# Optimization experiments

Measured on AMD Instinct MI355X. Metric: run time of the kernel, lower is better.

The kernel has to match this reference:

```python
import jax, jax.numpy as jnp
import numpy as np


def setup_inputs() -> dict:
    key = jax.random.key(0)
    k1, k2, k3 = jax.random.split(key, 3)
    B, M, J = 4096, 64, 24  # batch, n_max_markers, n_joints
    points = jax.random.normal(k1, (B, M, 3), dtype=jnp.float32)
    weight = jax.random.uniform(k2, (B, M, J), dtype=jnp.float32)  # positive soft weights
    offset = jax.random.normal(k3, (B, M, J, 3), dtype=jnp.float32)
    return {"points": points, "weight": weight, "offset": offset}


def reference(points, weight, offset):
    # P: per-joint marker offsets (B, J, 3, M); Q: world marker positions (B, 1, 3, M)
    P = jnp.transpose(offset, (0, 2, 3, 1))
    Q = jnp.transpose(points, (0, 2, 1))[:, None]
    w = jnp.transpose(weight, (0, 2, 1))[:, :, None]  # (B, J, 1, M)

    wsum = jnp.sum(w, axis=-1)                   # (B, J, 1)
    P_ = jnp.sum(P * w, axis=-1) / wsum          # (B, J, 3) weighted centroid of offsets
    Q_ = jnp.sum(Q * w, axis=-1) / wsum          # (B, J, 3) weighted centroid of markers

    X = P - P_[..., None]                        # (B, J, 3, M)
    Y = Q - Q_[..., None]                        # (B, J, 3, M) via broadcast

    # Cross-covariance S = X @ Y^T (NOTE: original multiplies un-weighted centered coords)
    S = jnp.einsum('bjdm,bjem->bjde', X, Y)      # (B, J, 3, 3)

    U, _, Vh = jnp.linalg.svd(S)
    V = jnp.swapaxes(Vh, -1, -2)
    Ut = jnp.swapaxes(U, -1, -2)
    det = jnp.linalg.det(jnp.matmul(V, Ut))      # (B, J) reflection correction
    Ut = Ut.at[..., -1, :].multiply(det[..., None])
    R = jnp.matmul(V, Ut)                        # (B, J, 3, 3) optimal rotation
    t = Q_[..., None] - jnp.matmul(R, P_[..., None])  # (B, J, 3, 1)
    return R, t
```

## Files before the change

### kernel.cpp

```cpp
#include <hip/hip_runtime.h>


constexpr int M = 64;
constexpr int J = 24;
constexpr int NACC = 22;
constexpr int NWS  = 15;
constexpr int WPB  = 2;

template<int P, int Q>
__device__ __forceinline__ void jrot(float A[4][4], float V[4][4]) {
    float apq = A[P][Q];
    float theta = (A[Q][Q] - A[P][P]) * __builtin_amdgcn_rcpf(2.0f * apq);
    float t = __builtin_amdgcn_rcpf(fabsf(theta) + __builtin_amdgcn_sqrtf(fmaf(theta, theta, 1.0f)));
    t = (theta < 0.0f) ? -t : t;
    t = (apq == 0.0f) ? 0.0f : t;
    float c = __builtin_amdgcn_rsqf(fmaf(t, t, 1.0f));
    float s = t * c;
#pragma unroll
    for (int k = 0; k < 4; ++k) {
        float akp = A[k][P], akq = A[k][Q];
        A[k][P] = c * akp - s * akq;
        A[k][Q] = s * akp + c * akq;
    }
#pragma unroll
    for (int k = 0; k < 4; ++k) {
        float apk = A[P][k], aqk = A[Q][k];
        A[P][k] = c * apk - s * aqk;
        A[Q][k] = s * apk + c * aqk;
        float vkp = V[k][P], vkq = V[k][Q];
        V[k][P] = c * vkp - s * vkq;
        V[k][Q] = s * vkp + c * vkq;
    }
}

__device__ __forceinline__ void horn_solve(
    float S00, float S01, float S02, float S10, float S11, float S12,
    float S20, float S21, float S22,
    float cP0, float cP1, float cP2, float cQ0, float cQ1, float cQ2,
    float* __restrict__ Rout, float* __restrict__ tout)
{
    float A[4][4], V[4][4];
    A[0][0] = S00 + S11 + S22;
    A[0][1] = A[1][0] = S12 - S21;
    A[0][2] = A[2][0] = S20 - S02;
    A[0][3] = A[3][0] = S01 - S10;
    A[1][1] = S00 - S11 - S22;
    A[1][2] = A[2][1] = S01 + S10;
    A[1][3] = A[3][1] = S02 + S20;
    A[2][2] = -S00 + S11 - S22;
    A[2][3] = A[3][2] = S12 + S21;
    A[3][3] = -S00 - S11 + S22;
#pragma unroll
    for (int r = 0; r < 4; ++r)
#pragma unroll
        for (int c = 0; c < 4; ++c)
            V[r][c] = (r == c) ? 1.0f : 0.0f;

#pragma unroll 1
    for (int sweep = 0; sweep < 6; ++sweep) {
        jrot<0, 1>(A, V); jrot<0, 2>(A, V); jrot<0, 3>(A, V);
        jrot<1, 2>(A, V); jrot<1, 3>(A, V); jrot<2, 3>(A, V);
    }

    float best = A[0][0];
    float qw = V[0][0], qx = V[1][0], qy = V[2][0], qz = V[3][0];
#pragma unroll
    for (int i = 1; i < 4; ++i) {
        bool better = A[i][i] > best;
        best = better ? A[i][i] : best;
        qw = better ? V[0][i] : qw;
        qx = better ? V[1][i] : qx;
        qy = better ? V[2][i] : qy;
        qz = better ? V[3][i] : qz;
    }
    float nrm = __builtin_amdgcn_rsqf(qw * qw + qx * qx + qy * qy + qz * qz);
    qw *= nrm; qx *= nrm; qy *= nrm; qz *= nrm;

    float R00 = 1.f - 2.f * (qy * qy + qz * qz);
    float R01 = 2.f * (qx * qy - qw * qz);
    float R02 = 2.f * (qx * qz + qw * qy);
    float R10 = 2.f * (qx * qy + qw * qz);
    float R11 = 1.f - 2.f * (qx * qx + qz * qz);
    float R12 = 2.f * (qy * qz - qw * qx);
    float R20 = 2.f * (qx * qz - qw * qy);
    float R21 = 2.f * (qy * qz + qw * qx);
    float R22 = 1.f - 2.f * (qx * qx + qy * qy);

    Rout[0] = R00; Rout[1] = R01; Rout[2] = R02;
    Rout[3] = R10; Rout[4] = R11; Rout[5] = R12;
    Rout[6] = R20; Rout[7] = R21; Rout[8] = R22;
    tout[0] = cQ0 - (R00 * cP0 + R01 * cP1 + R02 * cP2);
    tout[1] = cQ1 - (R10 * cP0 + R11 * cP1 + R12 * cP2);
    tout[2] = cQ2 - (R20 * cP0 + R21 * cP1 + R22 * cP2);
}

__global__ __launch_bounds__(128, 4) void kabsch_fused(
    const float* __restrict__ points,
    const float* __restrict__ weight,
    const float* __restrict__ offset,
    float* __restrict__ out,
    int B, int bj_total)
{
    const int t    = threadIdx.x;
    const int wv   = t >> 6;
    const int lane = t & 63;
    const int jj   = lane >> 1;
    const int kk   = lane & 1;

    int bw = blockIdx.x * WPB + wv;
    bw = bw < B ? bw : B - 1;

    __shared__ float sv_s[WPB][NWS][J + 1];

    if (jj < J) {
        const float* wq = weight + (size_t)bw * (M * J) + (size_t)(kk * 32) * J + jj;
        const float* oq = offset + (size_t)bw * (M * J * 3) + (size_t)(kk * 32) * (J * 3) + jj * 3;
        const float* pq = points + (size_t)bw * (M * 3) + (size_t)(kk * 32) * 3;

        float acc[NACC];
#pragma unroll
        for (int n = 0; n < NACC; ++n) acc[n] = 0.0f;

#pragma unroll
        for (int i = 0; i < M / 2; ++i) {
            float w  = wq[i * J];
            float o0 = oq[i * 72 + 0];
            float o1 = oq[i * 72 + 1];
            float o2 = oq[i * 72 + 2];
            float p0 = pq[i * 3 + 0];
            float p1 = pq[i * 3 + 1];
            float p2 = pq[i * 3 + 2];
            acc[0] += w;
            acc[1] = fmaf(w, o0, acc[1]);  acc[2] = fmaf(w, o1, acc[2]);  acc[3] = fmaf(w, o2, acc[3]);
            acc[4] = fmaf(w, p0, acc[4]);  acc[5] = fmaf(w, p1, acc[5]);  acc[6] = fmaf(w, p2, acc[6]);
            acc[7] += o0; acc[8] += o1; acc[9] += o2;
            acc[10] += p0; acc[11] += p1; acc[12] += p2;
            acc[13] = fmaf(o0, p0, acc[13]); acc[14] = fmaf(o0, p1, acc[14]); acc[15] = fmaf(o0, p2, acc[15]);
            acc[16] = fmaf(o1, p0, acc[16]); acc[17] = fmaf(o1, p1, acc[17]); acc[18] = fmaf(o1, p2, acc[18]);
            acc[19] = fmaf(o2, p0, acc[19]); acc[20] = fmaf(o2, p1, acc[20]); acc[21] = fmaf(o2, p2, acc[21]);
        }

#pragma unroll
        for (int n = 0; n < NACC; ++n) acc[n] += __shfl_xor(acc[n], 1);

        if (kk == 0) {
            const float inv = __builtin_amdgcn_rcpf(acc[0]);
            const float cP0 = acc[1] * inv, cP1 = acc[2] * inv, cP2 = acc[3] * inv;
            const float cQ0 = acc[4] * inv, cQ1 = acc[5] * inv, cQ2 = acc[6] * inv;
            const float To0 = acc[7], To1 = acc[8], To2 = acc[9];
            const float Tp0 = acc[10], Tp1 = acc[11], Tp2 = acc[12];
            const float fM = (float)M;
            sv_s[wv][0][jj]  = acc[13] - cP0 * Tp0 - cQ0 * To0 + fM * cP0 * cQ0;
            sv_s[wv][1][jj]  = acc[14] - cP0 * Tp1 - cQ1 * To0 + fM * cP0 * cQ1;
            sv_s[wv][2][jj]  = acc[15] - cP0 * Tp2 - cQ2 * To0 + fM * cP0 * cQ2;
            sv_s[wv][3][jj]  = acc[16] - cP1 * Tp0 - cQ0 * To1 + fM * cP1 * cQ0;
            sv_s[wv][4][jj]  = acc[17] - cP1 * Tp1 - cQ1 * To1 + fM * cP1 * cQ1;
            sv_s[wv][5][jj]  = acc[18] - cP1 * Tp2 - cQ2 * To1 + fM * cP1 * cQ2;
            sv_s[wv][6][jj]  = acc[19] - cP2 * Tp0 - cQ0 * To2 + fM * cP2 * cQ0;
            sv_s[wv][7][jj]  = acc[20] - cP2 * Tp1 - cQ1 * To2 + fM * cP2 * cQ1;
            sv_s[wv][8][jj]  = acc[21] - cP2 * Tp2 - cQ2 * To2 + fM * cP2 * cQ2;
            sv_s[wv][9][jj]  = cP0; sv_s[wv][10][jj] = cP1; sv_s[wv][11][jj] = cP2;
            sv_s[wv][12][jj] = cQ0; sv_s[wv][13][jj] = cQ1; sv_s[wv][14][jj] = cQ2;
        }
    }

    __syncthreads();

    if (t < WPB * J) {
        const int g  = t / J;
        const int j  = t - g * J;
        int bb = blockIdx.x * WPB + g;
        if (bb < B) {
            float v[NWS];
#pragma unroll
            for (int n = 0; n < NWS; ++n) v[n] = sv_s[g][n][j];
            float Rr[9], tr[3];
            horn_solve(v[0], v[1], v[2], v[3], v[4], v[5], v[6], v[7], v[8],
                       v[9], v[10], v[11], v[12], v[13], v[14], Rr, tr);
            const int bj = bb * J + j;
            float* Rout = out + (size_t)bj * 9;
#pragma unroll
            for (int n = 0; n < 9; ++n) Rout[n] = Rr[n];
            float* tout = out + (size_t)bj_total * 9 + (size_t)bj * 3;
            tout[0] = tr[0]; tout[1] = tr[1]; tout[2] = tr[2];
        }
    }
}

extern "C" void kernel_launch(void* const* d_in, const int* in_sizes, int n_in,
                              void* d_out, int out_size, void* d_ws, size_t ws_size,
                              hipStream_t stream) {
    const float* points = (const float*)d_in[0];
    const float* weight = (const float*)d_in[1];
    const float* offset = (const float*)d_in[2];
    float* out = (float*)d_out;

    int B = in_sizes[0] / (M * 3);
    int bj_total = B * J;
    int grid = (B + WPB - 1) / WPB;

    kabsch_fused<<<grid, 128, 0, stream>>>(points, weight, offset, out, B, bj_total);
}
```

Before: 140.2 us.

## Remap lanes to two joints and interleaved markers with float2 loads

Each lane now handles two adjacent joints and every fourth marker, where before it handled one joint and a contiguous half of the markers. Adjacent lanes therefore read adjacent memory, and the weight and offset loads become float2 vector loads. The point sums are shared across both joints, which cuts some redundant work. In exchange there are more accumulator registers (38+3) and a two-stage shuffle reduction, which could raise register pressure under launch bounds (128,4).

```diff
diff --git a/kernel.cpp b/kernel.cpp
--- a/kernel.cpp
+++ b/kernel.cpp
@@ -3,7 +3,6 @@
 
 constexpr int M = 64;
 constexpr int J = 24;
-constexpr int NACC = 22;
 constexpr int NWS  = 15;
 constexpr int WPB  = 2;
 
@@ -104,63 +103,92 @@
     const int t    = threadIdx.x;
     const int wv   = t >> 6;
     const int lane = t & 63;
-    const int jj   = lane >> 1;
-    const int kk   = lane & 1;
+    const int jp   = lane >> 2;
+    const int kq   = lane & 3;
 
     int bw = blockIdx.x * WPB + wv;
     bw = bw < B ? bw : B - 1;
 
     __shared__ float sv_s[WPB][NWS][J + 1];
 
-    if (jj < J) {
-        const float* wq = weight + (size_t)bw * (M * J) + (size_t)(kk * 32) * J + jj;
-        const float* oq = offset + (size_t)bw * (M * J * 3) + (size_t)(kk * 32) * (J * 3) + jj * 3;
-        const float* pq = points + (size_t)bw * (M * 3) + (size_t)(kk * 32) * 3;
-
-        float acc[NACC];
-#pragma unroll
-        for (int n = 0; n < NACC; ++n) acc[n] = 0.0f;
-
-#pragma unroll
-        for (int i = 0; i < M / 2; ++i) {
-            float w  = wq[i * J];
-            float o0 = oq[i * 72 + 0];
-            float o1 = oq[i * 72 + 1];
-            float o2 = oq[i * 72 + 2];
-            float p0 = pq[i * 3 + 0];
-            float p1 = pq[i * 3 + 1];
-            float p2 = pq[i * 3 + 2];
-            acc[0] += w;
-            acc[1] = fmaf(w, o0, acc[1]);  acc[2] = fmaf(w, o1, acc[2]);  acc[3] = fmaf(w, o2, acc[3]);
-            acc[4] = fmaf(w, p0, acc[4]);  acc[5] = fmaf(w, p1, acc[5]);  acc[6] = fmaf(w, p2, acc[6]);
-            acc[7] += o0; acc[8] += o1; acc[9] += o2;
-            acc[10] += p0; acc[11] += p1; acc[12] += p2;
-            acc[13] = fmaf(o0, p0, acc[13]); acc[14] = fmaf(o0, p1, acc[14]); acc[15] = fmaf(o0, p2, acc[15]);
-            acc[16] = fmaf(o1, p0, acc[16]); acc[17] = fmaf(o1, p1, acc[17]); acc[18] = fmaf(o1, p2, acc[18]);
-            acc[19] = fmaf(o2, p0, acc[19]); acc[20] = fmaf(o2, p1, acc[20]); acc[21] = fmaf(o2, p2, acc[21]);
+    if (jp < 12) {
+        const float* wq = weight + (size_t)bw * (M * J)     + kq * 24 + jp * 2;
+        const float* oq = offset + (size_t)bw * (M * J * 3) + kq * 72 + jp * 6;
+        const float* pq = points + (size_t)bw * (M * 3)     + kq * 3;
+
+        float ac[2][19];
+        float tp0 = 0.f, tp1 = 0.f, tp2 = 0.f;
+#pragma unroll
+        for (int jl = 0; jl < 2; ++jl)
+#pragma unroll
+            for (int n = 0; n < 19; ++n) ac[jl][n] = 0.f;
+
+#pragma unroll
+        for (int i = 0; i < 16; ++i) {
+            float2 w2 = *(const float2*)(wq + i * 96);
+            float2 oa = *(const float2*)(oq + i * 288);
+            float2 ob = *(const float2*)(oq + i * 288 + 2);
+            float2 oc = *(const float2*)(oq + i * 288 + 4);
+            float p0 = pq[i * 12 + 0];
+            float p1 = pq[i * 12 + 1];
+            float p2 = pq[i * 12 + 2];
+            tp0 += p0; tp1 += p1; tp2 += p2;
+            {
+                float w = w2.x, o0 = oa.x, o1 = oa.y, o2 = ob.x;
+                ac[0][0] += w;
+                ac[0][1] = fmaf(w, o0, ac[0][1]); ac[0][2] = fmaf(w, o1, ac[0][2]); ac[0][3] = fmaf(w, o2, ac[0][3]);
+                ac[0][4] = fmaf(w, p0, ac[0][4]); ac[0][5] = fmaf(w, p1, ac[0][5]); ac[0][6] = fmaf(w, p2, ac[0][6]);
+                ac[0][7] += o0; ac[0][8] += o1; ac[0][9] += o2;
+                ac[0][10] = fmaf(o0, p0, ac[0][10]); ac[0][11] = fmaf(o0, p1, ac[0][11]); ac[0][12] = fmaf(o0, p2, ac[0][12]);
+                ac[0][13] = fmaf(o1, p0, ac[0][13]); ac[0][14] = fmaf(o1, p1, ac[0][14]); ac[0][15] = fmaf(o1, p2, ac[0][15]);
+                ac[0][16] = fmaf(o2, p0, ac[0][16]); ac[0][17] = fmaf(o2, p1, ac[0][17]); ac[0][18] = fmaf(o2, p2, ac[0][18]);
+            }
+            {
+                float w = w2.y, o0 = ob.y, o1 = oc.x, o2 = oc.y;
+                ac[1][0] += w;
+                ac[1][1] = fmaf(w, o0, ac[1][1]); ac[1][2] = fmaf(w, o1, ac[1][2]); ac[1][3] = fmaf(w, o2, ac[1][3]);
+                ac[1][4] = fmaf(w, p0, ac[1][4]); ac[1][5] = fmaf(w, p1, ac[1][5]); ac[1][6] = fmaf(w, p2, ac[1][6]);
+                ac[1][7] += o0; ac[1][8] += o1; ac[1][9] += o2;
+                ac[1][10] = fmaf(o0, p0, ac[1][10]); ac[1][11] = fmaf(o0, p1, ac[1][11]); ac[1][12] = fmaf(o0, p2, ac[1][12]);
+                ac[1][13] = fmaf(o1, p0, ac[1][13]); ac[1][14] = fmaf(o1, p1, ac[1][14]); ac[1][15] = fmaf(o1, p2, ac[1][15]);
+                ac[1][16] = fmaf(o2, p0, ac[1][16]); ac[1][17] = fmaf(o2, p1, ac[1][17]); ac[1][18] = fmaf(o2, p2, ac[1][18]);
+            }
         }
 
 #pragma unroll
-        for (int n = 0; n < NACC; ++n) acc[n] += __shfl_xor(acc[n], 1);
-
-        if (kk == 0) {
-            const float inv = __builtin_amdgcn_rcpf(acc[0]);
-            const float cP0 = acc[1] * inv, cP1 = acc[2] * inv, cP2 = acc[3] * inv;
-            const float cQ0 = acc[4] * inv, cQ1 = acc[5] * inv, cQ2 = acc[6] * inv;
-            const float To0 = acc[7], To1 = acc[8], To2 = acc[9];
-            const float Tp0 = acc[10], Tp1 = acc[11], Tp2 = acc[12];
+        for (int jl = 0; jl < 2; ++jl)
+#pragma unroll
+            for (int n = 0; n < 19; ++n) {
+                float v = ac[jl][n];
+                v += __shfl_xor(v, 1);
+                v += __shfl_xor(v, 2);
+                ac[jl][n] = v;
+            }
+        tp0 += __shfl_xor(tp0, 1); tp0 += __shfl_xor(tp0, 2);
+        tp1 += __shfl_xor(tp1, 1); tp1 += __shfl_xor(tp1, 2);
+        tp2 += __shfl_xor(tp2, 1); tp2 += __shfl_xor(tp2, 2);
+
+        if (kq == 0) {
             const float fM = (float)M;
-            sv_s[wv][0][jj]  = acc[13] - cP0 * Tp0 - cQ0 * To0 + fM * cP0 * cQ0;
-            sv_s[wv][1][jj]  = acc[14] - cP0 * Tp1 - cQ1 * To0 + fM * cP0 * cQ1;
-            sv_s[wv][2][jj]  = acc[15] - cP0 * Tp2 - cQ2 * To0 + fM * cP0 * cQ2;
-            sv_s[wv][3][jj]  = acc[16] - cP1 * Tp0 - cQ0 * To1 + fM * cP1 * cQ0;
-            sv_s[wv][4][jj]  = acc[17] - cP1 * Tp1 - cQ1 * To1 + fM * cP1 * cQ1;
-            sv_s[wv][5][jj]  = acc[18] - cP1 * Tp2 - cQ2 * To1 + fM * cP1 * cQ2;
-            sv_s[wv][6][jj]  = acc[19] - cP2 * Tp0 - cQ0 * To2 + fM * cP2 * cQ0;
-            sv_s[wv][7][jj]  = acc[20] - cP2 * Tp1 - cQ1 * To2 + fM * cP2 * cQ1;
-            sv_s[wv][8][jj]  = acc[21] - cP2 * Tp2 - cQ2 * To2 + fM * cP2 * cQ2;
-            sv_s[wv][9][jj]  = cP0; sv_s[wv][10][jj] = cP1; sv_s[wv][11][jj] = cP2;
-            sv_s[wv][12][jj] = cQ0; sv_s[wv][13][jj] = cQ1; sv_s[wv][14][jj] = cQ2;
+#pragma unroll
+            for (int jl = 0; jl < 2; ++jl) {
+                const float inv = __builtin_amdgcn_rcpf(ac[jl][0]);
+                const float cP0 = ac[jl][1] * inv, cP1 = ac[jl][2] * inv, cP2 = ac[jl][3] * inv;
+                const float cQ0 = ac[jl][4] * inv, cQ1 = ac[jl][5] * inv, cQ2 = ac[jl][6] * inv;
+                const float To0 = ac[jl][7], To1 = ac[jl][8], To2 = ac[jl][9];
+                const int j = jp * 2 + jl;
+                sv_s[wv][0][j]  = ac[jl][10] - cP0 * tp0 - cQ0 * To0 + fM * cP0 * cQ0;
+                sv_s[wv][1][j]  = ac[jl][11] - cP0 * tp1 - cQ1 * To0 + fM * cP0 * cQ1;
+                sv_s[wv][2][j]  = ac[jl][12] - cP0 * tp2 - cQ2 * To0 + fM * cP0 * cQ2;
+                sv_s[wv][3][j]  = ac[jl][13] - cP1 * tp0 - cQ0 * To1 + fM * cP1 * cQ0;
+                sv_s[wv][4][j]  = ac[jl][14] - cP1 * tp1 - cQ1 * To1 + fM * cP1 * cQ1;
+                sv_s[wv][5][j]  = ac[jl][15] - cP1 * tp2 - cQ2 * To1 + fM * cP1 * cQ2;
+                sv_s[wv][6][j]  = ac[jl][16] - cP2 * tp0 - cQ0 * To2 + fM * cP2 * cQ0;
+                sv_s[wv][7][j]  = ac[jl][17] - cP2 * tp1 - cQ1 * To2 + fM * cP2 * cQ1;
+                sv_s[wv][8][j]  = ac[jl][18] - cP2 * tp2 - cQ2 * To2 + fM * cP2 * cQ2;
+                sv_s[wv][9][j]  = cP0; sv_s[wv][10][j] = cP1; sv_s[wv][11][j] = cP2;
+                sv_s[wv][12][j] = cQ0; sv_s[wv][13][j] = cQ1; sv_s[wv][14][j] = cQ2;
+            }
         }
     }
 
```

Measured after the change: 149.6 us. 6.7% more time.

## Split each batch's marker reduction across two waves with interleaved markers

Applied to the files above, without the earlier changes.

Each batch element is now reduced by two wavefronts instead of one, and the block grows to 256 threads. Each wave covers half of the markers. Markers are interleaved between the two lanes of a pair, so adjacent lanes read adjacent marker rows, which should improve coalescing. The per-thread serial loop is halved, which raises memory-level parallelism. The cost is an extra shared-memory partial-sum exchange and one more block barrier.

```diff
diff --git a/kernel.cpp b/kernel.cpp
--- a/kernel.cpp
+++ b/kernel.cpp
@@ -5,7 +5,7 @@
 constexpr int J = 24;
 constexpr int NACC = 22;
 constexpr int NWS  = 15;
-constexpr int WPB  = 2;
+constexpr int BPB  = 2;
 
 template<int P, int Q>
 __device__ __forceinline__ void jrot(float A[4][4], float V[4][4]) {
@@ -94,7 +94,7 @@
     tout[2] = cQ2 - (R20 * cP0 + R21 * cP1 + R22 * cP2);
 }
 
-__global__ __launch_bounds__(128, 4) void kabsch_fused(
+__global__ __launch_bounds__(256, 8) void kabsch_fused(
     const float* __restrict__ points,
     const float* __restrict__ weight,
     const float* __restrict__ offset,
@@ -103,33 +103,37 @@
 {
     const int t    = threadIdx.x;
     const int wv   = t >> 6;
+    const int g    = wv >> 1;
+    const int h    = wv & 1;
     const int lane = t & 63;
     const int jj   = lane >> 1;
     const int kk   = lane & 1;
 
-    int bw = blockIdx.x * WPB + wv;
+    int bw = blockIdx.x * BPB + g;
     bw = bw < B ? bw : B - 1;
 
-    __shared__ float sv_s[WPB][NWS][J + 1];
+    __shared__ float part[BPB][NACC][J + 1];
+    __shared__ float sv_s[BPB][NWS][J + 1];
+
+    float acc[NACC];
+#pragma unroll
+    for (int n = 0; n < NACC; ++n) acc[n] = 0.0f;
 
     if (jj < J) {
-        const float* wq = weight + (size_t)bw * (M * J) + (size_t)(kk * 32) * J + jj;
-        const float* oq = offset + (size_t)bw * (M * J * 3) + (size_t)(kk * 32) * (J * 3) + jj * 3;
-        const float* pq = points + (size_t)bw * (M * 3) + (size_t)(kk * 32) * 3;
-
-        float acc[NACC];
-#pragma unroll
-        for (int n = 0; n < NACC; ++n) acc[n] = 0.0f;
-
-#pragma unroll
-        for (int i = 0; i < M / 2; ++i) {
-            float w  = wq[i * J];
-            float o0 = oq[i * 72 + 0];
-            float o1 = oq[i * 72 + 1];
-            float o2 = oq[i * 72 + 2];
-            float p0 = pq[i * 3 + 0];
-            float p1 = pq[i * 3 + 1];
-            float p2 = pq[i * 3 + 2];
+        const int m0 = h * 32 + kk;
+        const float* wq = weight + (size_t)bw * (M * J)     + (size_t)m0 * J + jj;
+        const float* oq = offset + (size_t)bw * (M * J * 3) + (size_t)m0 * (J * 3) + jj * 3;
+        const float* pq = points + (size_t)bw * (M * 3)     + (size_t)m0 * 3;
+
+#pragma unroll
+        for (int i = 0; i < 16; ++i) {
+            float w  = wq[i * 48];
+            float o0 = oq[i * 144 + 0];
+            float o1 = oq[i * 144 + 1];
+            float o2 = oq[i * 144 + 2];
+            float p0 = pq[i * 6 + 0];
+            float p1 = pq[i * 6 + 1];
+            float p2 = pq[i * 6 + 2];
             acc[0] += w;
             acc[1] = fmaf(w, o0, acc[1]);  acc[2] = fmaf(w, o1, acc[2]);  acc[3] = fmaf(w, o2, acc[3]);
             acc[4] = fmaf(w, p0, acc[4]);  acc[5] = fmaf(w, p1, acc[5]);  acc[6] = fmaf(w, p2, acc[6]);
@@ -143,37 +147,47 @@
 #pragma unroll
         for (int n = 0; n < NACC; ++n) acc[n] += __shfl_xor(acc[n], 1);
 
-        if (kk == 0) {
-            const float inv = __builtin_amdgcn_rcpf(acc[0]);
-            const float cP0 = acc[1] * inv, cP1 = acc[2] * inv, cP2 = acc[3] * inv;
-            const float cQ0 = acc[4] * inv, cQ1 = acc[5] * inv, cQ2 = acc[6] * inv;
-            const float To0 = acc[7], To1 = acc[8], To2 = acc[9];
-            const float Tp0 = acc[10], Tp1 = acc[11], Tp2 = acc[12];
-            const float fM = (float)M;
-            sv_s[wv][0][jj]  = acc[13] - cP0 * Tp0 - cQ0 * To0 + fM * cP0 * cQ0;
-            sv_s[wv][1][jj]  = acc[14] - cP0 * Tp1 - cQ1 * To0 + fM * cP0 * cQ1;
-            sv_s[wv][2][jj]  = acc[15] - cP0 * Tp2 - cQ2 * To0 + fM * cP0 * cQ2;
-            sv_s[wv][3][jj]  = acc[16] - cP1 * Tp0 - cQ0 * To1 + fM * cP1 * cQ0;
-            sv_s[wv][4][jj]  = acc[17] - cP1 * Tp1 - cQ1 * To1 + fM * cP1 * cQ1;
-            sv_s[wv][5][jj]  = acc[18] - cP1 * Tp2 - cQ2 * To1 + fM * cP1 * cQ2;
-            sv_s[wv][6][jj]  = acc[19] - cP2 * Tp0 - cQ0 * To2 + fM * cP2 * cQ0;
-            sv_s[wv][7][jj]  = acc[20] - cP2 * Tp1 - cQ1 * To2 + fM * cP2 * cQ1;
-            sv_s[wv][8][jj]  = acc[21] - cP2 * Tp2 - cQ2 * To2 + fM * cP2 * cQ2;
-            sv_s[wv][9][jj]  = cP0; sv_s[wv][10][jj] = cP1; sv_s[wv][11][jj] = cP2;
-            sv_s[wv][12][jj] = cQ0; sv_s[wv][13][jj] = cQ1; sv_s[wv][14][jj] = cQ2;
+        if (h == 1 && kk == 0) {
+#pragma unroll
+            for (int n = 0; n < NACC; ++n) part[g][n][jj] = acc[n];
         }
     }
 
     __syncthreads();
 
-    if (t < WPB * J) {
-        const int g  = t / J;
-        const int j  = t - g * J;
-        int bb = blockIdx.x * WPB + g;
+    if (jj < J && h == 0 && kk == 0) {
+#pragma unroll
+        for (int n = 0; n < NACC; ++n) acc[n] += part[g][n][jj];
+
+        const float inv = __builtin_amdgcn_rcpf(acc[0]);
+        const float cP0 = acc[1] * inv, cP1 = acc[2] * inv, cP2 = acc[3] * inv;
+        const float cQ0 = acc[4] * inv, cQ1 = acc[5] * inv, cQ2 = acc[6] * inv;
+        const float To0 = acc[7], To1 = acc[8], To2 = acc[9];
+        const float Tp0 = acc[10], Tp1 = acc[11], Tp2 = acc[12];
+        const float fM = (float)M;
+        sv_s[g][0][jj]  = acc[13] - cP0 * Tp0 - cQ0 * To0 + fM * cP0 * cQ0;
+        sv_s[g][1][jj]  = acc[14] - cP0 * Tp1 - cQ1 * To0 + fM * cP0 * cQ1;
+        sv_s[g][2][jj]  = acc[15] - cP0 * Tp2 - cQ2 * To0 + fM * cP0 * cQ2;
+        sv_s[g][3][jj]  = acc[16] - cP1 * Tp0 - cQ0 * To1 + fM * cP1 * cQ0;
+        sv_s[g][4][jj]  = acc[17] - cP1 * Tp1 - cQ1 * To1 + fM * cP1 * cQ1;
+        sv_s[g][5][jj]  = acc[18] - cP1 * Tp2 - cQ2 * To1 + fM * cP1 * cQ2;
+        sv_s[g][6][jj]  = acc[19] - cP2 * Tp0 - cQ0 * To2 + fM * cP2 * cQ0;
+        sv_s[g][7][jj]  = acc[20] - cP2 * Tp1 - cQ1 * To2 + fM * cP2 * cQ1;
+        sv_s[g][8][jj]  = acc[21] - cP2 * Tp2 - cQ2 * To2 + fM * cP2 * cQ2;
+        sv_s[g][9][jj]  = cP0; sv_s[g][10][jj] = cP1; sv_s[g][11][jj] = cP2;
+        sv_s[g][12][jj] = cQ0; sv_s[g][13][jj] = cQ1; sv_s[g][14][jj] = cQ2;
+    }
+
+    __syncthreads();
+
+    if (t < BPB * J) {
+        const int gs = t / J;
+        const int j  = t - gs * J;
+        int bb = blockIdx.x * BPB + gs;
         if (bb < B) {
             float v[NWS];
 #pragma unroll
-            for (int n = 0; n < NWS; ++n) v[n] = sv_s[g][n][j];
+            for (int n = 0; n < NWS; ++n) v[n] = sv_s[gs][n][j];
             float Rr[9], tr[3];
             horn_solve(v[0], v[1], v[2], v[3], v[4], v[5], v[6], v[7], v[8],
                        v[9], v[10], v[11], v[12], v[13], v[14], Rr, tr);
@@ -197,7 +211,7 @@
 
     int B = in_sizes[0] / (M * 3);
     int bj_total = B * J;
-    int grid = (B + WPB - 1) / WPB;
-
-    kabsch_fused<<<grid, 128, 0, stream>>>(points, weight, offset, out, B, bj_total);
-}
+    int grid = (B + BPB - 1) / BPB;
+
+    kabsch_fused<<<grid, 256, 0, stream>>>(points, weight, offset, out, B, bj_total);
+}
```

New measurement: 234.2 us. 67.1% more time.
